# Kernel optimization log

Hardware: AMD Instinct MI355X
Metric: run time of the kernel (lower is better)

The kernel has to match this reference:

```python
import jax, jax.numpy as jnp
import numpy as np

VOCAB = 32000
DIM = 1024
CTX = 4          # local_context_size
EPS = 1e-6       # linear-attention denominator eps
LN_EPS = 1e-5    # LayerNorm eps


def setup_inputs() -> dict:
    key = jax.random.key(0)
    ks = jax.random.split(key, 12)
    s = 0.02
    inp = {
        "x": jax.random.randint(ks[0], (2, 2048), 0, VOCAB),
        "embedding": jax.random.normal(ks[1], (VOCAB, DIM), jnp.float32) * s,
        "Wq": jax.random.normal(ks[2], (DIM, DIM), jnp.float32) * s,
        "bq": jnp.zeros((DIM,), jnp.float32),
        "Wk": jax.random.normal(ks[3], (DIM, DIM), jnp.float32) * s,
        "bk": jnp.zeros((DIM,), jnp.float32),
        "Wv": jax.random.normal(ks[4], (DIM, DIM), jnp.float32) * s,
        "bv": jnp.zeros((DIM,), jnp.float32),
        "Wo": jax.random.normal(ks[5], (DIM, DIM), jnp.float32) * s,
        "bo": jnp.zeros((DIM,), jnp.float32),
        "ln_gamma": jnp.ones((DIM,), jnp.float32),
        "ln_beta": jnp.zeros((DIM,), jnp.float32),
        "Wout": jax.random.normal(ks[6], (DIM, VOCAB), jnp.float32) * s,
        "bout": jnp.zeros((VOCAB,), jnp.float32),
    }
    return inp


def _feature_map(x):
    # F.elu(x) + 1.0
    return jax.nn.elu(x) + 1.0


def _local_context_sum(emb):
    # sum of emb shifted right by 0..CTX-1 (zeros padded at front)
    out = emb
    for off in range(1, CTX):
        out = out + jnp.pad(emb, ((0, 0), (off, 0), (0, 0)))[:, :-off, :]
    return out


def reference(x, embedding, Wq, bq, Wk, bk, Wv, bv, Wo, bo,
              ln_gamma, ln_beta, Wout, bout):
    emb = embedding[x]                       # [B,S,D]
    emb = _local_context_sum(emb)

    q = _feature_map(emb @ Wq + bq)          # [B,S,D], strictly positive
    k = _feature_map(emb @ Wk + bk)
    v = emb @ Wv + bv

    S = emb.shape[1]
    # Causal linear attention. Equivalent to the per-step recurrence:
    #   num_t = q_t . (sum_{s<=t} k_s v_s^T);  den_t = q_t . (sum_{s<=t} k_s)
    scores = jnp.einsum("bsd,btd->bst", q, k)            # [B,S,S]
    mask = jnp.tril(jnp.ones((S, S), scores.dtype))
    scores = scores * mask
    num = jnp.einsum("bst,bte->bse", scores, v)          # [B,S,D]
    den = jnp.sum(scores, axis=-1, keepdims=True) + EPS  # [B,S,1]
    attn = num / den

    out = attn @ Wo + bo                     # dsra out_proj

    # LayerNorm
    mu = jnp.mean(out, axis=-1, keepdims=True)
    var = jnp.mean(jnp.square(out - mu), axis=-1, keepdims=True)
    out = (out - mu) * jax.lax.rsqrt(var + LN_EPS) * ln_gamma + ln_beta

    logits = out @ Wout + bout               # [B,S,VOCAB]
    return logits
```

## Files before the change

kernel.cpp:

```cpp
#include <hip/hip_runtime.h>
#include <cstddef>

#define DIM   1024
#define VOCAB 32000
#define BATCH 2
#define SEQ   2048
#define CTX   4
#define EPS_D 1e-6f
#define LN_EPS 1e-5f

typedef __bf16 bf16x8 __attribute__((ext_vector_type(8)));
typedef float  f32x4  __attribute__((ext_vector_type(4)));
typedef unsigned short ushortx8 __attribute__((ext_vector_type(8)));

__device__ __forceinline__ unsigned short f2bf(float f) {
    unsigned u = __float_as_uint(f);
    u += 0x7fffu + ((u >> 16) & 1u);
    return (unsigned short)(u >> 16);
}
__device__ __forceinline__ float bf2f(unsigned short h) {
    return __uint_as_float((unsigned)h << 16);
}

#define GL16(gp, lp) __builtin_amdgcn_global_load_lds(                        \
    (const __attribute__((address_space(1))) void*)(gp),                      \
    (__attribute__((address_space(3))) void*)(lp), 16, 0, 0)

__global__ __launch_bounds__(256)
void embed_split_kernel(const int* __restrict__ x,
                        const float* __restrict__ table,
                        ushort* __restrict__ eh,
                        ushort* __restrict__ el) {
    int bs = blockIdx.x;
    int b = bs >> 11;
    int s = bs & (SEQ - 1);
    int d = threadIdx.x * 4;
    float4 acc = make_float4(0.f, 0.f, 0.f, 0.f);
    #pragma unroll
    for (int o = 0; o < CTX; ++o) {
        int ss = s - o;
        if (ss >= 0) {
            int row = x[b * SEQ + ss];
            const float4 v = *(const float4*)&table[(size_t)row * DIM + d];
            acc.x += v.x; acc.y += v.y; acc.z += v.z; acc.w += v.w;
        }
    }
    ushort4 h, l;
    h.x = f2bf(acc.x); l.x = f2bf(acc.x - bf2f(h.x));
    h.y = f2bf(acc.y); l.y = f2bf(acc.y - bf2f(h.y));
    h.z = f2bf(acc.z); l.z = f2bf(acc.z - bf2f(h.z));
    h.w = f2bf(acc.w); l.w = f2bf(acc.w - bf2f(h.w));
    *(ushort4*)&eh[(size_t)bs * DIM + d] = h;
    *(ushort4*)&el[(size_t)bs * DIM + d] = l;
}

__global__ __launch_bounds__(256)
void embed_ctx_kernel(const int* __restrict__ x,
                      const float* __restrict__ table,
                      float* __restrict__ emb) {
    int bs = blockIdx.x;
    int b = bs >> 11;
    int s = bs & (SEQ - 1);
    int d = threadIdx.x * 4;
    float4 acc = make_float4(0.f, 0.f, 0.f, 0.f);
    #pragma unroll
    for (int o = 0; o < CTX; ++o) {
        int ss = s - o;
        if (ss >= 0) {
            int row = x[b * SEQ + ss];
            const float4 v = *(const float4*)&table[(size_t)row * DIM + d];
            acc.x += v.x; acc.y += v.y; acc.z += v.z; acc.w += v.w;
        }
    }
    *(float4*)&emb[(size_t)bs * DIM + d] = acc;
}

__device__ __forceinline__ void tsplit_body(const float* __restrict__ W,
                                            ushort* __restrict__ th,
                                            ushort* __restrict__ tl,
                                            int K, int N) {
    __shared__ float tile[32][129];
    const int n0 = blockIdx.x * 32;
    const int k0 = blockIdx.y * 128;
    const int t = threadIdx.x;

    #pragma unroll
    for (int it = 0; it < 4; ++it) {
        int kk = it * 32 + (t >> 3);
        int nn = (t & 7) * 4;
        float4 v4 = *(const float4*)&W[(size_t)(k0 + kk) * N + n0 + nn];
        tile[nn + 0][kk] = v4.x;
        tile[nn + 1][kk] = v4.y;
        tile[nn + 2][kk] = v4.z;
        tile[nn + 3][kk] = v4.w;
    }
    __syncthreads();

    #pragma unroll
    for (int it = 0; it < 2; ++it) {
        int u = it * 256 + t;
        int nn = u >> 4;
        int kc = (u & 15) * 8;
        ushortx8 h, l;
        #pragma unroll
        for (int j = 0; j < 8; ++j) {
            float f = tile[nn][kc + j];
            unsigned short hb = f2bf(f);
            h[j] = hb;
            l[j] = f2bf(f - bf2f(hb));
        }
        size_t off = (size_t)(n0 + nn) * K + k0 + kc;
        *(ushortx8*)&th[off] = h;
        *(ushortx8*)&tl[off] = l;
    }
}

__global__ __launch_bounds__(256)
void tsplit_kernel(const float* __restrict__ W,
                   ushort* __restrict__ th,
                   ushort* __restrict__ tl,
                   int K, int N) {
    tsplit_body(W, th, tl, K, N);
}

__global__ __launch_bounds__(256)
void tsplit4_kernel(const float* __restrict__ Wq, const float* __restrict__ Wk,
                    const float* __restrict__ Wv, const float* __restrict__ Wo,
                    ushort* __restrict__ qkvTh, ushort* __restrict__ qkvTl,
                    ushort* __restrict__ WoTh,  ushort* __restrict__ WoTl) {
    const int z = blockIdx.z;
    const float* W = (z == 0) ? Wq : (z == 1) ? Wk : (z == 2) ? Wv : Wo;
    ushort* th = (z < 3) ? qkvTh + (size_t)z * DIM * DIM : WoTh;
    ushort* tl = (z < 3) ? qkvTl + (size_t)z * DIM * DIM : WoTl;
    tsplit_body(W, th, tl, DIM, DIM);
}

template<int ACT, bool HASB, bool HASDIV, bool CAUSAL, bool TRIK, int OM>
__global__ __launch_bounds__(256, 2)
void mfma3_kernel(const ushort* __restrict__ Ah, const ushort* __restrict__ Al,
                  const ushort* __restrict__ Bh, const ushort* __restrict__ Bl,
                  const float* __restrict__ bias, const float* __restrict__ denp,
                  float* __restrict__ Cf, ushort* __restrict__ Ch, ushort* __restrict__ Cl,
                  int M, int N, int K,
                  long long aBat, long long bBat, long long cBat, long long dBat) {
    __shared__ __align__(16) ushort sAh[4096];
    __shared__ __align__(16) ushort sAl[4096];
    __shared__ __align__(16) ushort sBh[4096];
    __shared__ __align__(16) ushort sBl[4096];

    const int tid = threadIdx.x;
    const int zb = blockIdx.y;
    Ah += (size_t)zb * aBat;  Al += (size_t)zb * aBat;
    Bh += (size_t)zb * bBat;  Bl += (size_t)zb * bBat;
    if (OM == 0) { Cf += (size_t)zb * cBat; }
    else         { Ch += (size_t)zb * cBat; Cl += (size_t)zb * cBat; }
    if (HASDIV) denp += (size_t)zb * dBat;

    const int ntn = N >> 7;
    const int mbase = (blockIdx.x / ntn) << 7;
    const int nbase = (blockIdx.x % ntn) << 7;

    if (CAUSAL && nbase > mbase + 127) return;

    const int srl = tid >> 2;
    const int schunk = (tid & 3) ^ ((tid >> 3) & 3);
    const size_t skofs = (size_t)schunk * 8;

    const ushort* gAh0 = Ah + (size_t)(mbase + srl) * K + skofs;
    const ushort* gAh1 = Ah + (size_t)(mbase + 64 + srl) * K + skofs;
    const ushort* gAl0 = Al + (size_t)(mbase + srl) * K + skofs;
    const ushort* gAl1 = Al + (size_t)(mbase + 64 + srl) * K + skofs;
    const ushort* gBh0 = Bh + (size_t)(nbase + srl) * K + skofs;
    const ushort* gBh1 = Bh + (size_t)(nbase + 64 + srl) * K + skofs;
    const ushort* gBl0 = Bl + (size_t)(nbase + srl) * K + skofs;
    const ushort* gBl1 = Bl + (size_t)(nbase + 64 + srl) * K + skofs;

    const int l0 = tid * 8;
    const int l1 = 2048 + tid * 8;

    const int lane = tid & 63;
    const int wid = tid >> 6;
    const int wr = (wid >> 1) * 64;
    const int wc = (wid & 1) * 64;
    const int lrow = lane & 15;
    const int g = lane >> 4;
    int aoff[4], boff[4];
    #pragma unroll
    for (int i = 0; i < 4; ++i) {
        int r = wr + i * 16 + lrow;
        aoff[i] = r * 32 + ((g ^ ((r >> 1) & 3)) << 3);
        int rn = wc + i * 16 + lrow;
        boff[i] = rn * 32 + ((g ^ ((rn >> 1) & 3)) << 3);
    }

    f32x4 acc[4][4];
    #pragma unroll
    for (int i = 0; i < 4; ++i)
        #pragma unroll
        for (int j = 0; j < 4; ++j)
            acc[i][j] = (f32x4){0.f, 0.f, 0.f, 0.f};

    const int ktiles = TRIK ? ((mbase + 128) >> 5) : (K >> 5);
    for (int kt = 0; kt < ktiles; ++kt) {
        GL16(gAh0, sAh + l0);  GL16(gAh1, sAh + l1);
        GL16(gAl0, sAl + l0);  GL16(gAl1, sAl + l1);
        GL16(gBh0, sBh + l0);  GL16(gBh1, sBh + l1);
        GL16(gBl0, sBl + l0);  GL16(gBl1, sBl + l1);
        gAh0 += 32; gAh1 += 32; gAl0 += 32; gAl1 += 32;
        gBh0 += 32; gBh1 += 32; gBl0 += 32; gBl1 += 32;
        __syncthreads();

        bf16x8 fBh[4], fBl[4];
        #pragma unroll
        for (int i = 0; i < 4; ++i) {
            fBh[i] = *(const bf16x8*)(sBh + boff[i]);
            fBl[i] = *(const bf16x8*)(sBl + boff[i]);
        }
        #pragma unroll
        for (int mi = 0; mi < 4; ++mi) {
            bf16x8 ah = *(const bf16x8*)(sAh + aoff[mi]);
            bf16x8 al = *(const bf16x8*)(sAl + aoff[mi]);
            #pragma unroll
            for (int ni = 0; ni < 4; ++ni) {
                acc[mi][ni] = __builtin_amdgcn_mfma_f32_16x16x32_bf16(ah, fBh[ni], acc[mi][ni], 0, 0, 0);
                acc[mi][ni] = __builtin_amdgcn_mfma_f32_16x16x32_bf16(ah, fBl[ni], acc[mi][ni], 0, 0, 0);
                acc[mi][ni] = __builtin_amdgcn_mfma_f32_16x16x32_bf16(al, fBh[ni], acc[mi][ni], 0, 0, 0);
            }
        }
        __syncthreads();
    }

    #pragma unroll
    for (int ni = 0; ni < 4; ++ni) {
        const int c = nbase + wc + ni * 16 + lrow;
        float bv = 0.f;
        if (HASB) bv = bias[c];
        #pragma unroll
        for (int mi = 0; mi < 4; ++mi) {
            #pragma unroll
            for (int rg = 0; rg < 4; ++rg) {
                const int r = mbase + wr + mi * 16 + g * 4 + rg;
                float vv = acc[mi][ni][rg];
                if (HASDIV) vv /= denp[r];
                if (HASB) vv += bv;
                if (ACT == 1) vv = (vv > 0.f) ? (vv + 1.f) : __expf(vv);
                if (CAUSAL && c > r) vv = 0.f;
                if (OM == 0) {
                    Cf[(size_t)r * N + c] = vv;
                } else {
                    unsigned short hb = f2bf(vv);
                    Ch[(size_t)r * N + c] = hb;
                    Cl[(size_t)r * N + c] = f2bf(vv - bf2f(hb));
                }
            }
        }
    }
}

__global__ __launch_bounds__(256, 2)
void qkvproj_kernel(const ushort* __restrict__ Ah, const ushort* __restrict__ Al,
                    const ushort* __restrict__ Bh, const ushort* __restrict__ Bl,
                    const float* __restrict__ bq, const float* __restrict__ bk,
                    const float* __restrict__ bv_,
                    ushort* __restrict__ qh, ushort* __restrict__ ql,
                    ushort* __restrict__ kh, ushort* __restrict__ kl,
                    ushort* __restrict__ vTh, ushort* __restrict__ vTl) {
    __shared__ __align__(16) ushort sAh[4096];
    __shared__ __align__(16) ushort sAl[4096];
    __shared__ __align__(16) ushort sBh[4096];
    __shared__ __align__(16) ushort sBl[4096];

    const int tid = threadIdx.x;
    const int ntn = 24;
    const int mbase = (blockIdx.x / ntn) << 7;
    const int nbase = (blockIdx.x % ntn) << 7;
    const int mode = nbase >> 10;
    const int cb = nbase & 1023;

    const int srl = tid >> 2;
    const int schunk = (tid & 3) ^ ((tid >> 3) & 3);
    const size_t skofs = (size_t)schunk * 8;

    const ushort* gAh0 = Ah + (size_t)(mbase + srl) * DIM + skofs;
    const ushort* gAh1 = Ah + (size_t)(mbase + 64 + srl) * DIM + skofs;
    const ushort* gAl0 = Al + (size_t)(mbase + srl) * DIM + skofs;
    const ushort* gAl1 = Al + (size_t)(mbase + 64 + srl) * DIM + skofs;
    const ushort* gBh0 = Bh + (size_t)(nbase + srl) * DIM + skofs;
    const ushort* gBh1 = Bh + (size_t)(nbase + 64 + srl) * DIM + skofs;
    const ushort* gBl0 = Bl + (size_t)(nbase + srl) * DIM + skofs;
    const ushort* gBl1 = Bl + (size_t)(nbase + 64 + srl) * DIM + skofs;

    const int l0 = tid * 8;
    const int l1 = 2048 + tid * 8;

    const int lane = tid & 63;
    const int wid = tid >> 6;
    const int wr = (wid >> 1) * 64;
    const int wc = (wid & 1) * 64;
    const int lrow = lane & 15;
    const int g = lane >> 4;
    int aoff[4], boff[4];
    #pragma unroll
    for (int i = 0; i < 4; ++i) {
        int r = wr + i * 16 + lrow;
        aoff[i] = r * 32 + ((g ^ ((r >> 1) & 3)) << 3);
        int rn = wc + i * 16 + lrow;
        boff[i] = rn * 32 + ((g ^ ((rn >> 1) & 3)) << 3);
    }

    f32x4 acc[4][4];
    #pragma unroll
    for (int i = 0; i < 4; ++i)
        #pragma unroll
        for (int j = 0; j < 4; ++j)
            acc[i][j] = (f32x4){0.f, 0.f, 0.f, 0.f};

    for (int kt = 0; kt < DIM / 32; ++kt) {
        GL16(gAh0, sAh + l0);  GL16(gAh1, sAh + l1);
        GL16(gAl0, sAl + l0);  GL16(gAl1, sAl + l1);
        GL16(gBh0, sBh + l0);  GL16(gBh1, sBh + l1);
        GL16(gBl0, sBl + l0);  GL16(gBl1, sBl + l1);
        gAh0 += 32; gAh1 += 32; gAl0 += 32; gAl1 += 32;
        gBh0 += 32; gBh1 += 32; gBl0 += 32; gBl1 += 32;
        __syncthreads();

        bf16x8 fBh[4], fBl[4];
        #pragma unroll
        for (int i = 0; i < 4; ++i) {
            fBh[i] = *(const bf16x8*)(sBh + boff[i]);
            fBl[i] = *(const bf16x8*)(sBl + boff[i]);
        }
        #pragma unroll
        for (int mi = 0; mi < 4; ++mi) {
            bf16x8 ah = *(const bf16x8*)(sAh + aoff[mi]);
            bf16x8 al = *(const bf16x8*)(sAl + aoff[mi]);
            #pragma unroll
            for (int ni = 0; ni < 4; ++ni) {
                acc[mi][ni] = __builtin_amdgcn_mfma_f32_16x16x32_bf16(ah, fBh[ni], acc[mi][ni], 0, 0, 0);
                acc[mi][ni] = __builtin_amdgcn_mfma_f32_16x16x32_bf16(ah, fBl[ni], acc[mi][ni], 0, 0, 0);
                acc[mi][ni] = __builtin_amdgcn_mfma_f32_16x16x32_bf16(al, fBh[ni], acc[mi][ni], 0, 0, 0);
            }
        }
        __syncthreads();
    }

    const float* bias = (mode == 0) ? bq : (mode == 1) ? bk : bv_;
    ushort* dh = (mode == 0) ? qh : kh;
    ushort* dl = (mode == 0) ? ql : kl;

    #pragma unroll
    for (int ni = 0; ni < 4; ++ni) {
        const int c = cb + wc + ni * 16 + lrow;
        const float bvv = bias[c];
        #pragma unroll
        for (int mi = 0; mi < 4; ++mi) {
            if (mode < 2) {
                #pragma unroll
                for (int rg = 0; rg < 4; ++rg) {
                    const int r = mbase + wr + mi * 16 + g * 4 + rg;
                    float vv = acc[mi][ni][rg] + bvv;
                    vv = (vv > 0.f) ? (vv + 1.f) : __expf(vv);
                    unsigned short hb = f2bf(vv);
                    dh[(size_t)r * DIM + c] = hb;
                    dl[(size_t)r * DIM + c] = f2bf(vv - bf2f(hb));
                }
            } else {
                const int r0 = mbase + wr + mi * 16 + g * 4;
                const int batch = r0 >> 11;
                const int s0 = r0 & (SEQ - 1);
                ushort4 h4, l4;
                #pragma unroll
                for (int rg = 0; rg < 4; ++rg) {
                    float vv = acc[mi][ni][rg] + bvv;
                    unsigned short hb = f2bf(vv);
                    ((unsigned short*)&h4)[rg] = hb;
                    ((unsigned short*)&l4)[rg] = f2bf(vv - bf2f(hb));
                }
                size_t off = (size_t)batch * DIM * SEQ + (size_t)c * SEQ + s0;
                *(ushort4*)&vTh[off] = h4;
                *(ushort4*)&vTl[off] = l4;
            }
        }
    }
}

__device__ __forceinline__ float block_reduce_sum(float v, float* red) {
    #pragma unroll
    for (int off = 32; off > 0; off >>= 1) v += __shfl_down(v, off);
    const int lane = threadIdx.x & 63;
    const int wid = threadIdx.x >> 6;
    if (lane == 0) red[wid] = v;
    __syncthreads();
    float s = red[0] + red[1] + red[2] + red[3];
    return s;
}

__global__ __launch_bounds__(256)
void den_bf_kernel(const ushort* __restrict__ sh,
                   const ushort* __restrict__ sl,
                   float* __restrict__ den) {
    const int row = blockIdx.x;
    const int b = row >> 11;
    const int i = row & (SEQ - 1);
    const size_t base = (size_t)b * SEQ * SEQ + (size_t)i * SEQ;
    const int j = threadIdx.x * 8;
    ushortx8 h = *(const ushortx8*)&sh[base + j];
    ushortx8 l = *(const ushortx8*)&sl[base + j];
    float s = 0.f;
    int lim = i - j;
    if (lim > 7) lim = 7;
    for (int t = 0; t <= lim; ++t) s += bf2f(h[t]) + bf2f(l[t]);
    __shared__ float red[4];
    float tot = block_reduce_sum(s, red);
    if (threadIdx.x == 0) den[row] = tot + EPS_D;
}

__global__ __launch_bounds__(256)
void den_kernel(const float* __restrict__ scores, float* __restrict__ den) {
    const int row = blockIdx.x;
    const int b = row >> 11;
    const int i = row & (SEQ - 1);
    const float* r = scores + (size_t)b * SEQ * SEQ + (size_t)i * SEQ;
    float s = 0.f;
    for (int j = threadIdx.x * 4; j < SEQ; j += 256 * 4) {
        float4 v = *(const float4*)&r[j];
        s += v.x + v.y + v.z + v.w;
    }
    __shared__ float red[4];
    float tot = block_reduce_sum(s, red);
    if (threadIdx.x == 0) den[row] = tot + EPS_D;
}

__global__ __launch_bounds__(256)
void ln_split_kernel(const float* __restrict__ io,
                     const float* __restrict__ gamma,
                     const float* __restrict__ beta,
                     ushort* __restrict__ ahi,
                     ushort* __restrict__ alo) {
    const size_t row = blockIdx.x;
    const float* r = io + row * DIM;
    const int d = threadIdx.x * 4;
    float4 v = *(const float4*)&r[d];
    float s = v.x + v.y + v.z + v.w;
    float sq = v.x * v.x + v.y * v.y + v.z * v.z + v.w * v.w;
    __shared__ float r1[4];
    __shared__ float r2[4];
    float tot = block_reduce_sum(s, r1);
    __syncthreads();
    float totsq = block_reduce_sum(sq, r2);
    const float mu = tot * (1.f / DIM);
    const float var = totsq * (1.f / DIM) - mu * mu;
    const float rs = rsqrtf(var + LN_EPS);
    float4 gv = *(const float4*)&gamma[d];
    float4 bv = *(const float4*)&beta[d];
    v.x = (v.x - mu) * rs * gv.x + bv.x;
    v.y = (v.y - mu) * rs * gv.y + bv.y;
    v.z = (v.z - mu) * rs * gv.z + bv.z;
    v.w = (v.w - mu) * rs * gv.w + bv.w;
    ushort4 h, l;
    h.x = f2bf(v.x); l.x = f2bf(v.x - bf2f(h.x));
    h.y = f2bf(v.y); l.y = f2bf(v.y - bf2f(h.y));
    h.z = f2bf(v.z); l.z = f2bf(v.z - bf2f(h.z));
    h.w = f2bf(v.w); l.w = f2bf(v.w - bf2f(h.w));
    *(ushort4*)&ahi[row * DIM + d] = h;
    *(ushort4*)&alo[row * DIM + d] = l;
}

__global__ __launch_bounds__(256)
void ln_kernel(float* __restrict__ io,
               const float* __restrict__ gamma,
               const float* __restrict__ beta) {
    const size_t row = blockIdx.x;
    float* r = io + row * DIM;
    const int d = threadIdx.x * 4;
    float4 v = *(const float4*)&r[d];
    float s = v.x + v.y + v.z + v.w;
    float sq = v.x * v.x + v.y * v.y + v.z * v.z + v.w * v.w;
    __shared__ float r1[4];
    __shared__ float r2[4];
    float tot = block_reduce_sum(s, r1);
    __syncthreads();
    float totsq = block_reduce_sum(sq, r2);
    const float mu = tot * (1.f / DIM);
    const float var = totsq * (1.f / DIM) - mu * mu;
    const float rs = rsqrtf(var + LN_EPS);
    float4 gv = *(const float4*)&gamma[d];
    float4 bv = *(const float4*)&beta[d];
    v.x = (v.x - mu) * rs * gv.x + bv.x;
    v.y = (v.y - mu) * rs * gv.y + bv.y;
    v.z = (v.z - mu) * rs * gv.z + bv.z;
    v.w = (v.w - mu) * rs * gv.w + bv.w;
    *(float4*)&r[d] = v;
}

__global__ __launch_bounds__(256, 2)
void logits_mfma_kernel(const ushort* __restrict__ Ahi,
                        const ushort* __restrict__ Alo,
                        const ushort* __restrict__ Bhi,
                        const ushort* __restrict__ Blo,
                        const float* __restrict__ bias,
                        float* __restrict__ C) {
    __shared__ __align__(16) ushort sAh[4096];
    __shared__ __align__(16) ushort sAl[4096];
    __shared__ __align__(16) ushort sBh[4096];
    __shared__ __align__(16) ushort sBl[4096];

    const int tid = threadIdx.x;
    const int bid = blockIdx.x;
    const int xcd = bid & 7;
    const int idx = bid >> 3;
    const int mbase = ((xcd << 2) | (idx & 3)) * 128;
    const int nbase = (idx >> 2) * 128;

    const int srl = tid >> 2;
    const int schunk = (tid & 3) ^ ((tid >> 3) & 3);
    const size_t skofs = (size_t)schunk * 8;

    const ushort* gAh0 = Ahi + (size_t)(mbase + srl) * DIM + skofs;
    const ushort* gAh1 = Ahi + (size_t)(mbase + 64 + srl) * DIM + skofs;
    const ushort* gAl0 = Alo + (size_t)(mbase + srl) * DIM + skofs;
    const ushort* gAl1 = Alo + (size_t)(mbase + 64 + srl) * DIM + skofs;
    const ushort* gBh0 = Bhi + (size_t)(nbase + srl) * DIM + skofs;
    const ushort* gBh1 = Bhi + (size_t)(nbase + 64 + srl) * DIM + skofs;
    const ushort* gBl0 = Blo + (size_t)(nbase + srl) * DIM + skofs;
    const ushort* gBl1 = Blo + (size_t)(nbase + 64 + srl) * DIM + skofs;

    const int l0 = tid * 8;
    const int l1 = 2048 + tid * 8;

    const int lane = tid & 63;
    const int wid = tid >> 6;
    const int wr = (wid >> 1) * 64;
    const int wc = (wid & 1) * 64;
    const int lrow = lane & 15;
    const int g = lane >> 4;
    int aoff[4], boff[4];
    #pragma unroll
    for (int i = 0; i < 4; ++i) {
        int r = wr + i * 16 + lrow;
        aoff[i] = r * 32 + ((g ^ ((r >> 1) & 3)) << 3);
        int rn = wc + i * 16 + lrow;
        boff[i] = rn * 32 + ((g ^ ((rn >> 1) & 3)) << 3);
    }

    f32x4 acc[4][4];
    #pragma unroll
    for (int i = 0; i < 4; ++i)
        #pragma unroll
        for (int j = 0; j < 4; ++j)
            acc[i][j] = (f32x4){0.f, 0.f, 0.f, 0.f};

    for (int kt = 0; kt < DIM / 32; ++kt) {
        GL16(gAh0, sAh + l0);  GL16(gAh1, sAh + l1);
        GL16(gAl0, sAl + l0);  GL16(gAl1, sAl + l1);
        GL16(gBh0, sBh + l0);  GL16(gBh1, sBh + l1);
        GL16(gBl0, sBl + l0);  GL16(gBl1, sBl + l1);
        gAh0 += 32; gAh1 += 32; gAl0 += 32; gAl1 += 32;
        gBh0 += 32; gBh1 += 32; gBl0 += 32; gBl1 += 32;
        __syncthreads();

        bf16x8 fBh[4], fBl[4];
        #pragma unroll
        for (int i = 0; i < 4; ++i) {
            fBh[i] = *(const bf16x8*)(sBh + boff[i]);
            fBl[i] = *(const bf16x8*)(sBl + boff[i]);
        }
        #pragma unroll
        for (int mi = 0; mi < 4; ++mi) {
            bf16x8 ah = *(const bf16x8*)(sAh + aoff[mi]);
            bf16x8 al = *(const bf16x8*)(sAl + aoff[mi]);
            #pragma unroll
            for (int ni = 0; ni < 4; ++ni) {
                acc[mi][ni] = __builtin_amdgcn_mfma_f32_16x16x32_bf16(ah, fBh[ni], acc[mi][ni], 0, 0, 0);
                acc[mi][ni] = __builtin_amdgcn_mfma_f32_16x16x32_bf16(ah, fBl[ni], acc[mi][ni], 0, 0, 0);
                acc[mi][ni] = __builtin_amdgcn_mfma_f32_16x16x32_bf16(al, fBh[ni], acc[mi][ni], 0, 0, 0);
            }
        }
        __syncthreads();
    }

    #pragma unroll
    for (int ni = 0; ni < 4; ++ni) {
        const int c = nbase + wc + ni * 16 + lrow;
        const float bv = bias[c];
        #pragma unroll
        for (int mi = 0; mi < 4; ++mi) {
            #pragma unroll
            for (int rg = 0; rg < 4; ++rg) {
                const int r = mbase + wr + mi * 16 + g * 4 + rg;
                __builtin_nontemporal_store(acc[mi][ni][rg] + bv,
                                            &C[(size_t)r * VOCAB + c]);
            }
        }
    }
}

template<int ACT, bool HAS_BIAS, bool HAS_DIV>
__global__ __launch_bounds__(256)
void gemm_kernel(const float* __restrict__ A,
                 const float* __restrict__ B,
                 const float* __restrict__ bias,
                 const float* __restrict__ rowdiv,
                 float* __restrict__ C,
                 int M, int N, int K) {
    __shared__ float As[16][64];
    __shared__ float Bs[16][64];

    const int tid = threadIdx.x;
    const int tx = tid & 15;
    const int ty = tid >> 4;
    const int row0 = blockIdx.y * 64;
    const int col0 = blockIdx.x * 64;

    const int a_row = tid >> 2;
    const int a_col = (tid & 3) * 4;
    const int b_row = tid >> 4;
    const int b_col = (tid & 15) * 4;

    const float* Aptr = A + (size_t)(row0 + a_row) * K + a_col;
    const float* Bptr = B + (size_t)b_row * N + col0 + b_col;

    float acc[4][4];
    #pragma unroll
    for (int i = 0; i < 4; ++i)
        #pragma unroll
        for (int j = 0; j < 4; ++j) acc[i][j] = 0.f;

    for (int k0 = 0; k0 < K; k0 += 16) {
        float4 a4 = *(const float4*)(Aptr + k0);
        float4 b4 = *(const float4*)(Bptr + (size_t)k0 * N);
        As[a_col + 0][a_row] = a4.x;
        As[a_col + 1][a_row] = a4.y;
        As[a_col + 2][a_row] = a4.z;
        As[a_col + 3][a_row] = a4.w;
        *(float4*)&Bs[b_row][b_col] = b4;
        __syncthreads();
        #pragma unroll
        for (int kk = 0; kk < 16; ++kk) {
            float4 av = *(const float4*)&As[kk][ty * 4];
            float4 bv = *(const float4*)&Bs[kk][tx * 4];
            float am[4] = {av.x, av.y, av.z, av.w};
            float bm[4] = {bv.x, bv.y, bv.z, bv.w};
            #pragma unroll
            for (int i = 0; i < 4; ++i)
                #pragma unroll
                for (int j = 0; j < 4; ++j)
                    acc[i][j] = fmaf(am[i], bm[j], acc[i][j]);
        }
        __syncthreads();
    }

    #pragma unroll
    for (int i = 0; i < 4; ++i) {
        const int r = row0 + ty * 4 + i;
        float rdiv = 1.f;
        if (HAS_DIV) rdiv = 1.f / rowdiv[r];
        #pragma unroll
        for (int j = 0; j < 4; ++j) {
            const int c = col0 + tx * 4 + j;
            float v = acc[i][j] * rdiv;
            if (HAS_BIAS) v += bias[c];
            if (ACT == 1) v = (v > 0.f) ? (v + 1.f) : __expf(v);
            C[(size_t)r * N + c] = v;
        }
    }
}

__global__ __launch_bounds__(256)
void scores_kernel(const float* __restrict__ q,
                   const float* __restrict__ k,
                   float* __restrict__ scores) {
    const int b = blockIdx.z;
    const int tid = threadIdx.x;
    const int tx = tid & 15;
    const int ty = tid >> 4;
    const int i0 = blockIdx.y * 64;
    const int j0 = blockIdx.x * 64;
    float* Sc = scores + (size_t)b * SEQ * SEQ;

    if (j0 > i0 + 63) {
        #pragma unroll
        for (int i = 0; i < 4; ++i)
            #pragma unroll
            for (int j = 0; j < 4; ++j)
                Sc[(size_t)(i0 + ty * 4 + i) * SEQ + j0 + tx * 4 + j] = 0.f;
        return;
    }

    const float* Q = q + (size_t)b * SEQ * DIM;
    const float* Kp = k + (size_t)b * SEQ * DIM;

    __shared__ float Qs[16][64];
    __shared__ float Ks[16][64];

    const int l_row = tid >> 2;
    const int l_col = (tid & 3) * 4;

    const float* Qptr = Q + (size_t)(i0 + l_row) * DIM + l_col;
    const float* Kptr = Kp + (size_t)(j0 + l_row) * DIM + l_col;

    float acc[4][4];
    #pragma unroll
    for (int i = 0; i < 4; ++i)
        #pragma unroll
        for (int j = 0; j < 4; ++j) acc[i][j] = 0.f;

    for (int d0 = 0; d0 < DIM; d0 += 16) {
        float4 a4 = *(const float4*)(Qptr + d0);
        float4 b4 = *(const float4*)(Kptr + d0);
        Qs[l_col + 0][l_row] = a4.x;
        Qs[l_col + 1][l_row] = a4.y;
        Qs[l_col + 2][l_row] = a4.z;
        Qs[l_col + 3][l_row] = a4.w;
        Ks[l_col + 0][l_row] = b4.x;
        Ks[l_col + 1][l_row] = b4.y;
        Ks[l_col + 2][l_row] = b4.z;
        Ks[l_col + 3][l_row] = b4.w;
        __syncthreads();
        #pragma unroll
        for (int kk = 0; kk < 16; ++kk) {
            float4 av = *(const float4*)&Qs[kk][ty * 4];
            float4 bv = *(const float4*)&Ks[kk][tx * 4];
            float am[4] = {av.x, av.y, av.z, av.w};
            float bm[4] = {bv.x, bv.y, bv.z, bv.w};
            #pragma unroll
            for (int i = 0; i < 4; ++i)
                #pragma unroll
                for (int j = 0; j < 4; ++j)
                    acc[i][j] = fmaf(am[i], bm[j], acc[i][j]);
        }
        __syncthreads();
    }

    #pragma unroll
    for (int i = 0; i < 4; ++i) {
        const int ii = i0 + ty * 4 + i;
        #pragma unroll
        for (int j = 0; j < 4; ++j) {
            const int jj = j0 + tx * 4 + j;
            Sc[(size_t)ii * SEQ + jj] = (jj <= ii) ? acc[i][j] : 0.f;
        }
    }
}

extern "C" void kernel_launch(void* const* d_in, const int* in_sizes, int n_in,
                              void* d_out, int out_size, void* d_ws, size_t ws_size,
                              hipStream_t stream) {
    const int*   x     = (const int*)d_in[0];
    const float* table = (const float*)d_in[1];
    const float* Wq    = (const float*)d_in[2];
    const float* bq    = (const float*)d_in[3];
    const float* Wk    = (const float*)d_in[4];
    const float* bk    = (const float*)d_in[5];
    const float* Wv    = (const float*)d_in[6];
    const float* bv    = (const float*)d_in[7];
    const float* Wo    = (const float*)d_in[8];
    const float* bo    = (const float*)d_in[9];
    const float* gamma = (const float*)d_in[10];
    const float* beta  = (const float*)d_in[11];
    const float* Wout  = (const float*)d_in[12];
    const float* bout  = (const float*)d_in[13];
    float* logits = (float*)d_out;

    const int M = BATCH * SEQ;

    char* p = (char*)d_ws;
    auto alloc = [&](size_t bytes) { char* r = p; p += bytes; return r; };
    ushort* WoutTh = (ushort*)alloc((size_t)VOCAB * DIM * 2);
    ushort* WoutTl = (ushort*)alloc((size_t)VOCAB * DIM * 2);
    ushort* ehi    = (ushort*)alloc((size_t)M * DIM * 2);
    ushort* elo    = (ushort*)alloc((size_t)M * DIM * 2);
    ushort* WqkvTh = (ushort*)alloc((size_t)3 * DIM * DIM * 2);
    ushort* WqkvTl = (ushort*)alloc((size_t)3 * DIM * DIM * 2);
    ushort* WoTh   = (ushort*)alloc((size_t)DIM * DIM * 2);
    ushort* WoTl   = (ushort*)alloc((size_t)DIM * DIM * 2);
    ushort* qhi    = (ushort*)alloc((size_t)M * DIM * 2);
    ushort* qlo    = (ushort*)alloc((size_t)M * DIM * 2);
    ushort* khi    = (ushort*)alloc((size_t)M * DIM * 2);
    ushort* klo    = (ushort*)alloc((size_t)M * DIM * 2);
    ushort* vTh    = (ushort*)alloc((size_t)BATCH * DIM * SEQ * 2);
    ushort* vTl    = (ushort*)alloc((size_t)BATCH * DIM * SEQ * 2);
    ushort* shi    = (ushort*)alloc((size_t)BATCH * SEQ * SEQ * 2);
    ushort* slo    = (ushort*)alloc((size_t)BATCH * SEQ * SEQ * 2);
    float*  den    = (float*)alloc((size_t)M * 4);
    const size_t need = (size_t)(p - (char*)d_ws);

    ushort* attnh = qhi;
    ushort* attnl = qlo;
    float*  outf  = (float*)khi;
    ushort* ahi   = ehi;
    ushort* alo   = elo;

    if (ws_size >= need) {
        tsplit4_kernel<<<dim3(DIM / 32, DIM / 128, 4), 256, 0, stream>>>(
            Wq, Wk, Wv, Wo, WqkvTh, WqkvTl, WoTh, WoTl);
        tsplit_kernel<<<dim3(VOCAB / 32, DIM / 128), 256, 0, stream>>>(
            Wout, WoutTh, WoutTl, DIM, VOCAB);

        embed_split_kernel<<<M, 256, 0, stream>>>(x, table, ehi, elo);

        qkvproj_kernel<<<(M / 128) * 24, 256, 0, stream>>>(
            ehi, elo, WqkvTh, WqkvTl, bq, bk, bv,
            qhi, qlo, khi, klo, vTh, vTl);

        mfma3_kernel<0, false, false, true, false, 1>
            <<<dim3((SEQ / 128) * (SEQ / 128), BATCH), 256, 0, stream>>>(
            qhi, qlo, khi, klo, nullptr, nullptr, nullptr, shi, slo,
            SEQ, SEQ, DIM,
            (long long)SEQ * DIM, (long long)SEQ * DIM, (long long)SEQ * SEQ, 0);
        den_bf_kernel<<<M, 256, 0, stream>>>(shi, slo, den);

        mfma3_kernel<0, false, true, false, true, 1>
            <<<dim3((SEQ / 128) * (DIM / 128), BATCH), 256, 0, stream>>>(
            shi, slo, vTh, vTl, nullptr, den, nullptr, attnh, attnl,
            SEQ, DIM, SEQ,
            (long long)SEQ * SEQ, (long long)DIM * SEQ, (long long)SEQ * DIM,
            (long long)SEQ);

        mfma3_kernel<0, true, false, false, false, 0>
            <<<dim3((M / 128) * (DIM / 128), 1), 256, 0, stream>>>(
            attnh, attnl, WoTh, WoTl, bo, nullptr, outf, nullptr, nullptr,
            M, DIM, DIM, 0, 0, 0, 0);

        ln_split_kernel<<<M, 256, 0, stream>>>(outf, gamma, beta, ahi, alo);

        logits_mfma_kernel<<<(M / 128) * (VOCAB / 128), 256, 0, stream>>>(
            ahi, alo, WoutTh, WoutTl, bout, logits);
    } else {
        const size_t NE = (size_t)M * DIM;
        float* ws    = (float*)d_ws;
        float* emb   = ws;
        float* q     = ws + NE;
        float* k     = ws + 2 * NE;
        float* v     = ws + 3 * NE;
        float* sc    = ws + 4 * NE;
        float* denf  = sc + (size_t)BATCH * SEQ * SEQ;
        float* attn  = emb;
        float* out   = q;

        embed_ctx_kernel<<<M, 256, 0, stream>>>(x, table, emb);
        dim3 gq(DIM / 64, M / 64);
        gemm_kernel<1, true, false><<<gq, 256, 0, stream>>>(emb, Wq, bq, nullptr, q, M, DIM, DIM);
        gemm_kernel<1, true, false><<<gq, 256, 0, stream>>>(emb, Wk, bk, nullptr, k, M, DIM, DIM);
        gemm_kernel<0, true, false><<<gq, 256, 0, stream>>>(emb, Wv, bv, nullptr, v, M, DIM, DIM);
        dim3 gs(SEQ / 64, SEQ / 64, BATCH);
        scores_kernel<<<gs, 256, 0, stream>>>(q, k, sc);
        den_kernel<<<M, 256, 0, stream>>>(sc, denf);
        dim3 gn(DIM / 64, SEQ / 64);
        for (int b = 0; b < BATCH; ++b) {
            gemm_kernel<0, false, true><<<gn, 256, 0, stream>>>(
                sc + (size_t)b * SEQ * SEQ, v + (size_t)b * SEQ * DIM,
                nullptr, denf + (size_t)b * SEQ,
                attn + (size_t)b * SEQ * DIM, SEQ, DIM, SEQ);
        }
        gemm_kernel<0, true, false><<<gq, 256, 0, stream>>>(attn, Wo, bo, nullptr, out, M, DIM, DIM);
        ln_kernel<<<M, 256, 0, stream>>>(out, gamma, beta);
        dim3 gl(VOCAB / 64, M / 64);
        gemm_kernel<0, true, false><<<gl, 256, 0, stream>>>(out, Wout, bout, nullptr, logits, M, VOCAB, DIM);
    }
}
```

Baseline: 1.584 ms.

## Stage GEMM epilogues through LDS, fuse row-sum denominator, merge weight-split launches

Makes the bf16 hi/lo output epilogues of the score GEMM and QKV projection stage through swizzled LDS so global stores are coalesced 16-byte vectors, including the transposed V layout. The causal score GEMM now sums each tile's rows and atomically adds the sums into the denominator, which the embedding kernel initialises to eps, so the separate den_bf kernel goes away. The two weight-transpose-split kernels are merged into one launch. The exchange is extra LDS round trips and barriers in the epilogue, plus atomics that make the denominator's summation order nondeterministic.

```diff
diff --git a/kernel.cpp b/kernel.cpp
--- a/kernel.cpp
+++ b/kernel.cpp
@@ -30,11 +30,13 @@
 void embed_split_kernel(const int* __restrict__ x,
                         const float* __restrict__ table,
                         ushort* __restrict__ eh,
-                        ushort* __restrict__ el) {
+                        ushort* __restrict__ el,
+                        float* __restrict__ den) {
     int bs = blockIdx.x;
     int b = bs >> 11;
     int s = bs & (SEQ - 1);
     int d = threadIdx.x * 4;
+    if (threadIdx.x == 0) den[bs] = EPS_D;
     float4 acc = make_float4(0.f, 0.f, 0.f, 0.f);
     #pragma unroll
     for (int o = 0; o < CTX; ++o) {
@@ -78,10 +80,8 @@
 __device__ __forceinline__ void tsplit_body(const float* __restrict__ W,
                                             ushort* __restrict__ th,
                                             ushort* __restrict__ tl,
-                                            int K, int N) {
+                                            int K, int N, int n0, int k0) {
     __shared__ float tile[32][129];
-    const int n0 = blockIdx.x * 32;
-    const int k0 = blockIdx.y * 128;
     const int t = threadIdx.x;
 
     #pragma unroll
@@ -116,37 +116,41 @@
 }
 
 __global__ __launch_bounds__(256)
-void tsplit_kernel(const float* __restrict__ W,
-                   ushort* __restrict__ th,
-                   ushort* __restrict__ tl,
-                   int K, int N) {
-    tsplit_body(W, th, tl, K, N);
-}
-
-__global__ __launch_bounds__(256)
-void tsplit4_kernel(const float* __restrict__ Wq, const float* __restrict__ Wk,
-                    const float* __restrict__ Wv, const float* __restrict__ Wo,
-                    ushort* __restrict__ qkvTh, ushort* __restrict__ qkvTl,
-                    ushort* __restrict__ WoTh,  ushort* __restrict__ WoTl) {
-    const int z = blockIdx.z;
-    const float* W = (z == 0) ? Wq : (z == 1) ? Wk : (z == 2) ? Wv : Wo;
-    ushort* th = (z < 3) ? qkvTh + (size_t)z * DIM * DIM : WoTh;
-    ushort* tl = (z < 3) ? qkvTl + (size_t)z * DIM * DIM : WoTl;
-    tsplit_body(W, th, tl, DIM, DIM);
-}
-
-template<int ACT, bool HASB, bool HASDIV, bool CAUSAL, bool TRIK, int OM>
+void wsplit_all_kernel(const float* __restrict__ Wq, const float* __restrict__ Wk,
+                       const float* __restrict__ Wv, const float* __restrict__ Wo,
+                       const float* __restrict__ Wout,
+                       ushort* __restrict__ qkvTh, ushort* __restrict__ qkvTl,
+                       ushort* __restrict__ WoTh,  ushort* __restrict__ WoTl,
+                       ushort* __restrict__ WoutTh, ushort* __restrict__ WoutTl) {
+    const int bid = blockIdx.x;
+    if (bid < 8000) {
+        tsplit_body(Wout, WoutTh, WoutTl, DIM, VOCAB,
+                    (bid % 1000) * 32, (bid / 1000) * 128);
+    } else {
+        const int r = bid - 8000;
+        const int z = r >> 8;
+        const int rr = r & 255;
+        const float* W = (z == 0) ? Wq : (z == 1) ? Wk : (z == 2) ? Wv : Wo;
+        ushort* th = (z < 3) ? qkvTh + (size_t)z * DIM * DIM : WoTh;
+        ushort* tl = (z < 3) ? qkvTl + (size_t)z * DIM * DIM : WoTl;
+        tsplit_body(W, th, tl, DIM, DIM, (rr & 31) * 32, (rr >> 5) * 128);
+    }
+}
+
+template<int ACT, bool HASB, bool HASDIV, bool CAUSAL, bool TRIK, bool SUMROWS, int OM>
 __global__ __launch_bounds__(256, 2)
 void mfma3_kernel(const ushort* __restrict__ Ah, const ushort* __restrict__ Al,
                   const ushort* __restrict__ Bh, const ushort* __restrict__ Bl,
                   const float* __restrict__ bias, const float* __restrict__ denp,
+                  float* __restrict__ denout,
                   float* __restrict__ Cf, ushort* __restrict__ Ch, ushort* __restrict__ Cl,
                   int M, int N, int K,
                   long long aBat, long long bBat, long long cBat, long long dBat) {
-    __shared__ __align__(16) ushort sAh[4096];
-    __shared__ __align__(16) ushort sAl[4096];
-    __shared__ __align__(16) ushort sBh[4096];
-    __shared__ __align__(16) ushort sBl[4096];
+    __shared__ __align__(16) ushort sU[16384];
+    ushort* sAh = sU;
+    ushort* sAl = sU + 4096;
+    ushort* sBh = sU + 8192;
+    ushort* sBl = sU + 12288;
 
     const int tid = threadIdx.x;
     const int zb = blockIdx.y;
@@ -155,6 +159,7 @@
     if (OM == 0) { Cf += (size_t)zb * cBat; }
     else         { Ch += (size_t)zb * cBat; Cl += (size_t)zb * cBat; }
     if (HASDIV) denp += (size_t)zb * dBat;
+    if (SUMROWS) denout += (size_t)zb * dBat;
 
     const int ntn = N >> 7;
     const int mbase = (blockIdx.x / ntn) << 7;
@@ -230,30 +235,95 @@
         __syncthreads();
     }
 
-    #pragma unroll
-    for (int ni = 0; ni < 4; ++ni) {
-        const int c = nbase + wc + ni * 16 + lrow;
-        float bv = 0.f;
-        if (HASB) bv = bias[c];
-        #pragma unroll
-        for (int mi = 0; mi < 4; ++mi) {
-            #pragma unroll
-            for (int rg = 0; rg < 4; ++rg) {
-                const int r = mbase + wr + mi * 16 + g * 4 + rg;
-                float vv = acc[mi][ni][rg];
-                if (HASDIV) vv /= denp[r];
-                if (HASB) vv += bv;
-                if (ACT == 1) vv = (vv > 0.f) ? (vv + 1.f) : __expf(vv);
-                if (CAUSAL && c > r) vv = 0.f;
-                if (OM == 0) {
+    if (OM == 0) {
+        #pragma unroll
+        for (int ni = 0; ni < 4; ++ni) {
+            const int c = nbase + wc + ni * 16 + lrow;
+            float bv = 0.f;
+            if (HASB) bv = bias[c];
+            #pragma unroll
+            for (int mi = 0; mi < 4; ++mi) {
+                #pragma unroll
+                for (int rg = 0; rg < 4; ++rg) {
+                    const int r = mbase + wr + mi * 16 + g * 4 + rg;
+                    float vv = acc[mi][ni][rg];
+                    if (HASDIV) vv /= denp[r];
+                    if (HASB) vv += bv;
+                    if (ACT == 1) vv = (vv > 0.f) ? (vv + 1.f) : __expf(vv);
                     Cf[(size_t)r * N + c] = vv;
-                } else {
+                }
+            }
+        }
+    } else {
+        #pragma unroll
+        for (int ni = 0; ni < 4; ++ni) {
+            const int cl = wc + ni * 16 + lrow;
+            const int c = nbase + cl;
+            float bv = 0.f;
+            if (HASB) bv = bias[c];
+            #pragma unroll
+            for (int mi = 0; mi < 4; ++mi) {
+                #pragma unroll
+                for (int rg = 0; rg < 4; ++rg) {
+                    const int rl = wr + mi * 16 + g * 4 + rg;
+                    const int r = mbase + rl;
+                    float vv = acc[mi][ni][rg];
+                    if (HASDIV) vv /= denp[r];
+                    if (HASB) vv += bv;
+                    if (ACT == 1) vv = (vv > 0.f) ? (vv + 1.f) : __expf(vv);
+                    if (CAUSAL && c > r) vv = 0.f;
                     unsigned short hb = f2bf(vv);
-                    Ch[(size_t)r * N + c] = hb;
-                    Cl[(size_t)r * N + c] = f2bf(vv - bf2f(hb));
+                    sU[rl * 128 + (cl ^ ((rl & 15) << 3))] = hb;
+                    acc[mi][ni][rg] = vv - bf2f(hb);
                 }
             }
         }
+        __syncthreads();
+        const int orow = tid >> 1;
+        const int ohalf = (tid & 1) << 6;
+        const int oswz = (orow & 15) << 3;
+        float rsum = 0.f;
+        {
+            const size_t gb = (size_t)(mbase + orow) * N + nbase;
+            #pragma unroll
+            for (int j = 0; j < 8; ++j) {
+                const int cc = ohalf + j * 8;
+                ushortx8 v8 = *(const ushortx8*)&sU[orow * 128 + (cc ^ oswz)];
+                *(ushortx8*)&Ch[gb + cc] = v8;
+                if (SUMROWS) {
+                    #pragma unroll
+                    for (int t = 0; t < 8; ++t) rsum += bf2f(v8[t]);
+                }
+            }
+        }
+        __syncthreads();
+        #pragma unroll
+        for (int ni = 0; ni < 4; ++ni) {
+            const int cl = wc + ni * 16 + lrow;
+            #pragma unroll
+            for (int mi = 0; mi < 4; ++mi) {
+                #pragma unroll
+                for (int rg = 0; rg < 4; ++rg) {
+                    const int rl = wr + mi * 16 + g * 4 + rg;
+                    sU[rl * 128 + (cl ^ ((rl & 15) << 3))] = f2bf(acc[mi][ni][rg]);
+                }
+            }
+        }
+        __syncthreads();
+        {
+            const size_t gb = (size_t)(mbase + orow) * N + nbase;
+            #pragma unroll
+            for (int j = 0; j < 8; ++j) {
+                const int cc = ohalf + j * 8;
+                ushortx8 v8 = *(const ushortx8*)&sU[orow * 128 + (cc ^ oswz)];
+                *(ushortx8*)&Cl[gb + cc] = v8;
+                if (SUMROWS) {
+                    #pragma unroll
+                    for (int t = 0; t < 8; ++t) rsum += bf2f(v8[t]);
+                }
+            }
+        }
+        if (SUMROWS) atomicAdd(&denout[mbase + orow], rsum);
     }
 }
 
@@ -265,10 +335,11 @@
                     ushort* __restrict__ qh, ushort* __restrict__ ql,
                     ushort* __restrict__ kh, ushort* __restrict__ kl,
                     ushort* __restrict__ vTh, ushort* __restrict__ vTl) {
-    __shared__ __align__(16) ushort sAh[4096];
-    __shared__ __align__(16) ushort sAl[4096];
-    __shared__ __align__(16) ushort sBh[4096];
-    __shared__ __align__(16) ushort sBl[4096];
+    __shared__ __align__(16) ushort sU[16384];
+    ushort* sAh = sU;
+    ushort* sAl = sU + 4096;
+    ushort* sBh = sU + 8192;
+    ushort* sBl = sU + 12288;
 
     const int tid = threadIdx.x;
     const int ntn = 24;
@@ -345,40 +416,118 @@
     }
 
     const float* bias = (mode == 0) ? bq : (mode == 1) ? bk : bv_;
-    ushort* dh = (mode == 0) ? qh : kh;
-    ushort* dl = (mode == 0) ? ql : kl;
-
-    #pragma unroll
-    for (int ni = 0; ni < 4; ++ni) {
-        const int c = cb + wc + ni * 16 + lrow;
-        const float bvv = bias[c];
-        #pragma unroll
-        for (int mi = 0; mi < 4; ++mi) {
-            if (mode < 2) {
+
+    if (mode < 2) {
+        ushort* dh = (mode == 0) ? qh : kh;
+        ushort* dl = (mode == 0) ? ql : kl;
+        #pragma unroll
+        for (int ni = 0; ni < 4; ++ni) {
+            const int cl = wc + ni * 16 + lrow;
+            const float bvv = bias[cb + cl];
+            #pragma unroll
+            for (int mi = 0; mi < 4; ++mi) {
                 #pragma unroll
                 for (int rg = 0; rg < 4; ++rg) {
-                    const int r = mbase + wr + mi * 16 + g * 4 + rg;
+                    const int rl = wr + mi * 16 + g * 4 + rg;
                     float vv = acc[mi][ni][rg] + bvv;
                     vv = (vv > 0.f) ? (vv + 1.f) : __expf(vv);
                     unsigned short hb = f2bf(vv);
-                    dh[(size_t)r * DIM + c] = hb;
-                    dl[(size_t)r * DIM + c] = f2bf(vv - bf2f(hb));
+                    sU[rl * 128 + (cl ^ ((rl & 15) << 3))] = hb;
+                    acc[mi][ni][rg] = vv - bf2f(hb);
                 }
-            } else {
-                const int r0 = mbase + wr + mi * 16 + g * 4;
-                const int batch = r0 >> 11;
-                const int s0 = r0 & (SEQ - 1);
-                ushort4 h4, l4;
+            }
+        }
+        __syncthreads();
+        const int orow = tid >> 1;
+        const int ohalf = (tid & 1) << 6;
+        const int oswz = (orow & 15) << 3;
+        {
+            const size_t gb = (size_t)(mbase + orow) * DIM + cb;
+            #pragma unroll
+            for (int j = 0; j < 8; ++j) {
+                const int cc = ohalf + j * 8;
+                *(ushortx8*)&dh[gb + cc] =
+                    *(const ushortx8*)&sU[orow * 128 + (cc ^ oswz)];
+            }
+        }
+        __syncthreads();
+        #pragma unroll
+        for (int ni = 0; ni < 4; ++ni) {
+            const int cl = wc + ni * 16 + lrow;
+            #pragma unroll
+            for (int mi = 0; mi < 4; ++mi) {
                 #pragma unroll
                 for (int rg = 0; rg < 4; ++rg) {
+                    const int rl = wr + mi * 16 + g * 4 + rg;
+                    sU[rl * 128 + (cl ^ ((rl & 15) << 3))] = f2bf(acc[mi][ni][rg]);
+                }
+            }
+        }
+        __syncthreads();
+        {
+            const size_t gb = (size_t)(mbase + orow) * DIM + cb;
+            #pragma unroll
+            for (int j = 0; j < 8; ++j) {
+                const int cc = ohalf + j * 8;
+                *(ushortx8*)&dl[gb + cc] =
+                    *(const ushortx8*)&sU[orow * 128 + (cc ^ oswz)];
+            }
+        }
+    } else {
+        #pragma unroll
+        for (int ni = 0; ni < 4; ++ni) {
+            const int cl = wc + ni * 16 + lrow;
+            const float bvv = bias[cb + cl];
+            #pragma unroll
+            for (int mi = 0; mi < 4; ++mi) {
+                #pragma unroll
+                for (int rg = 0; rg < 4; ++rg) {
+                    const int rl = wr + mi * 16 + g * 4 + rg;
                     float vv = acc[mi][ni][rg] + bvv;
                     unsigned short hb = f2bf(vv);
-                    ((unsigned short*)&h4)[rg] = hb;
-                    ((unsigned short*)&l4)[rg] = f2bf(vv - bf2f(hb));
+                    sU[cl * 128 + (rl ^ ((cl & 15) << 3))] = hb;
+                    acc[mi][ni][rg] = vv - bf2f(hb);
                 }
-                size_t off = (size_t)batch * DIM * SEQ + (size_t)c * SEQ + s0;
-                *(ushort4*)&vTh[off] = h4;
-                *(ushort4*)&vTl[off] = l4;
+            }
+        }
+        __syncthreads();
+        const int ocol = tid >> 1;
+        const int ohalf = (tid & 1) << 6;
+        const int oswz = (ocol & 15) << 3;
+        const int batch = mbase >> 11;
+        const int s0 = mbase & (SEQ - 1);
+        {
+            const size_t gb = (size_t)batch * DIM * SEQ
+                            + (size_t)(cb + ocol) * SEQ + s0;
+            #pragma unroll
+            for (int j = 0; j < 8; ++j) {
+                const int rr = ohalf + j * 8;
+                *(ushortx8*)&vTh[gb + rr] =
+                    *(const ushortx8*)&sU[ocol * 128 + (rr ^ oswz)];
+            }
+        }
+        __syncthreads();
+        #pragma unroll
+        for (int ni = 0; ni < 4; ++ni) {
+            const int cl = wc + ni * 16 + lrow;
+            #pragma unroll
+            for (int mi = 0; mi < 4; ++mi) {
+                #pragma unroll
+                for (int rg = 0; rg < 4; ++rg) {
+                    const int rl = wr + mi * 16 + g * 4 + rg;
+                    sU[cl * 128 + (rl ^ ((cl & 15) << 3))] = f2bf(acc[mi][ni][rg]);
+                }
+            }
+        }
+        __syncthreads();
+        {
+            const size_t gb = (size_t)batch * DIM * SEQ
+                            + (size_t)(cb + ocol) * SEQ + s0;
+            #pragma unroll
+            for (int j = 0; j < 8; ++j) {
+                const int rr = ohalf + j * 8;
+                *(ushortx8*)&vTl[gb + rr] =
+                    *(const ushortx8*)&sU[ocol * 128 + (rr ^ oswz)];
             }
         }
     }
@@ -393,26 +542,6 @@
     __syncthreads();
     float s = red[0] + red[1] + red[2] + red[3];
     return s;
-}
-
-__global__ __launch_bounds__(256)
-void den_bf_kernel(const ushort* __restrict__ sh,
-                   const ushort* __restrict__ sl,
-                   float* __restrict__ den) {
-    const int row = blockIdx.x;
-    const int b = row >> 11;
-    const int i = row & (SEQ - 1);
-    const size_t base = (size_t)b * SEQ * SEQ + (size_t)i * SEQ;
-    const int j = threadIdx.x * 8;
-    ushortx8 h = *(const ushortx8*)&sh[base + j];
-    ushortx8 l = *(const ushortx8*)&sl[base + j];
-    float s = 0.f;
-    int lim = i - j;
-    if (lim > 7) lim = 7;
-    for (int t = 0; t <= lim; ++t) s += bf2f(h[t]) + bf2f(l[t]);
-    __shared__ float red[4];
-    float tot = block_reduce_sum(s, red);
-    if (threadIdx.x == 0) den[row] = tot + EPS_D;
 }
 
 __global__ __launch_bounds__(256)
@@ -792,34 +921,32 @@
     ushort* alo   = elo;
 
     if (ws_size >= need) {
-        tsplit4_kernel<<<dim3(DIM / 32, DIM / 128, 4), 256, 0, stream>>>(
-            Wq, Wk, Wv, Wo, WqkvTh, WqkvTl, WoTh, WoTl);
-        tsplit_kernel<<<dim3(VOCAB / 32, DIM / 128), 256, 0, stream>>>(
-            Wout, WoutTh, WoutTl, DIM, VOCAB);
-
-        embed_split_kernel<<<M, 256, 0, stream>>>(x, table, ehi, elo);
+        wsplit_all_kernel<<<8000 + 1024, 256, 0, stream>>>(
+            Wq, Wk, Wv, Wo, Wout, WqkvTh, WqkvTl, WoTh, WoTl, WoutTh, WoutTl);
+
+        embed_split_kernel<<<M, 256, 0, stream>>>(x, table, ehi, elo, den);
 
         qkvproj_kernel<<<(M / 128) * 24, 256, 0, stream>>>(
             ehi, elo, WqkvTh, WqkvTl, bq, bk, bv,
             qhi, qlo, khi, klo, vTh, vTl);
 
-        mfma3_kernel<0, false, false, true, false, 1>
+        mfma3_kernel<0, false, false, true, false, true, 1>
             <<<dim3((SEQ / 128) * (SEQ / 128), BATCH), 256, 0, stream>>>(
-            qhi, qlo, khi, klo, nullptr, nullptr, nullptr, shi, slo,
+            qhi, qlo, khi, klo, nullptr, nullptr, den, nullptr, shi, slo,
             SEQ, SEQ, DIM,
-            (long long)SEQ * DIM, (long long)SEQ * DIM, (long long)SEQ * SEQ, 0);
-        den_bf_kernel<<<M, 256, 0, stream>>>(shi, slo, den);
-
-        mfma3_kernel<0, false, true, false, true, 1>
+            (long long)SEQ * DIM, (long long)SEQ * DIM, (long long)SEQ * SEQ,
+            (long long)SEQ);
+
+        mfma3_kernel<0, false, true, false, true, false, 1>
             <<<dim3((SEQ / 128) * (DIM / 128), BATCH), 256, 0, stream>>>(
-            shi, slo, vTh, vTl, nullptr, den, nullptr, attnh, attnl,
+            shi, slo, vTh, vTl, nullptr, den, nullptr, nullptr, attnh, attnl,
             SEQ, DIM, SEQ,
             (long long)SEQ * SEQ, (long long)DIM * SEQ, (long long)SEQ * DIM,
             (long long)SEQ);
 
-        mfma3_kernel<0, true, false, false, false, 0>
+        mfma3_kernel<0, true, false, false, false, false, 0>
             <<<dim3((M / 128) * (DIM / 128), 1), 256, 0, stream>>>(
-            attnh, attnl, WoTh, WoTl, bo, nullptr, outf, nullptr, nullptr,
+            attnh, attnl, WoTh, WoTl, bo, nullptr, nullptr, outf, nullptr, nullptr,
             M, DIM, DIM, 0, 0, 0, 0);
 
         ln_split_kernel<<<M, 256, 0, stream>>>(outf, gamma, beta, ahi, alo);
```

Result: slower. 1.635 ms (+3.3%).
